# Optimization experiments

Measured on AMD Instinct MI355X. Metric: run time of the kernel, lower is better.

Reference implementation:

```python
import jax, jax.numpy as jnp
import numpy as np

K = 3          # kernel size
PAD = 1        # padding
KK = K * K
RECURRENT = 3  # opt.Recurrent_times - 1


def dcnv2(x, offset, mask, weight, bias):
    """Modulated deformable conv (DCNv2), stride 1, pad 1, dilation 1.

    x:      [B, C, H, W]
    offset: [B, 2*KK, H, W]  -- (dy, dx) interleaved per kernel tap
    mask:   [B, KK, H, W]    -- modulation scalars
    weight: [O, C, K, K], bias: [O]
    """
    B, C, H, W = x.shape
    off = offset.reshape(B, KK, 2, H, W)
    dy, dx = off[:, :, 0], off[:, :, 1]                       # [B,KK,H,W]

    ky, kx = jnp.meshgrid(jnp.arange(K), jnp.arange(K), indexing='ij')
    ky = (ky.reshape(KK) - PAD).astype(x.dtype)               # {-1,0,1}
    kx = (kx.reshape(KK) - PAD).astype(x.dtype)
    iy = jnp.arange(H, dtype=x.dtype)
    ix = jnp.arange(W, dtype=x.dtype)

    # fractional sampling coords, [B,KK,H,W]
    py = iy[None, None, :, None] + ky[None, :, None, None] + dy
    px = ix[None, None, None, :] + kx[None, :, None, None] + dx

    y0 = jnp.floor(py)
    x0 = jnp.floor(px)
    wy = (py - y0)[:, None]                                   # [B,1,KK,H,W]
    wx = (px - x0)[:, None]

    x_flat = x.reshape(B, C, H * W)

    def gather(yi, xi):
        valid = ((yi >= 0) & (yi <= H - 1) & (xi >= 0) & (xi <= W - 1))
        yc = jnp.clip(yi, 0, H - 1).astype(jnp.int32)
        xc = jnp.clip(xi, 0, W - 1).astype(jnp.int32)
        idx = (yc * W + xc).reshape(B, -1)                    # [B, KK*H*W]
        g = jax.vmap(lambda im, id_: im[:, id_])(x_flat, idx)  # [B,C,KK*H*W]
        return g.reshape(B, C, KK, H, W) * valid.astype(x.dtype)[:, None]

    v00 = gather(y0, x0)
    v01 = gather(y0, x0 + 1)
    v10 = gather(y0 + 1, x0)
    v11 = gather(y0 + 1, x0 + 1)

    val = (v00 * (1 - wy) * (1 - wx) + v01 * (1 - wy) * wx
           + v10 * wy * (1 - wx) + v11 * wy * wx)
    val = val * mask[:, None]                                  # modulation

    out = jnp.einsum('ock,bckhw->bohw', weight.reshape(weight.shape[0], C, KK), val)
    return out + bias[None, :, None, None]


def setup_inputs() -> dict:
    key = jax.random.key(0)
    k1, k2, k3 = jax.random.split(key, 3)
    B, H, W = 4, 512, 512
    sharp = jax.random.normal(k1, (B, 3, H, W), dtype=jnp.float32)
    motion = jax.random.normal(k2, (B, 3 * KK, H, W), dtype=jnp.float32)
    # one 3x3x3->3 conv per recurrence, stacked: [RECURRENT, O, C, K, K]
    dcn_weights = jax.random.normal(k3, (RECURRENT, 3, 3, K, K), dtype=jnp.float32) * 0.1
    dcn_biases = jnp.zeros((RECURRENT, 3), dtype=jnp.float32)
    return {"sharp": sharp, "motion": motion,
            "dcn_weights": dcn_weights, "dcn_biases": dcn_biases}


def reference(sharp, motion, dcn_weights, dcn_biases):
    # torch.split(motion, [2*KK, KK], dim=1)
    offset = motion[:, :2 * KK]
    mask = motion[:, 2 * KK:]
    feats = [sharp]
    cur = sharp
    for i in range(RECURRENT):
        cur = dcnv2(cur, offset, mask, dcn_weights[i], dcn_biases[i])
        feats.append(cur)
    return sum(feats) / (RECURRENT + 1)
```

## Files before the change

kernel.cpp:

```cpp
#include <hip/hip_runtime.h>
#include <hip/hip_fp16.h>


#define HH 512
#define WW 512
#define BATCH 4
#define HWSZ (HH * WW)
#define MP 28
#define MBLKS (108 * 256)

union U4 { uint4 u; __half2 h[4]; };
union U2 { uint2 u; __half2 h[2]; };

typedef const __attribute__((address_space(1))) void* gas_t;
typedef __attribute__((address_space(3))) void* las_t;

__global__ __launch_bounds__(256) void prep_kernel(
    const float* __restrict__ sharp, const float* __restrict__ motion,
    uint4* __restrict__ sharp16, __half* __restrict__ mot16)
{
    const int blk = blockIdx.x;
    const int t = threadIdx.x;
    if (blk < MBLKS) {
        const int P = blk >> 8;
        const int b = P / 27;
        const int pl = P - b * 27;
        const int off = (blk & 255) * 1024 + t * 4;
        const float4 v = *(const float4*)(motion + ((size_t)P << 18) + off);
        U2 o;
        o.h[0] = __float22half2_rn(make_float2(v.x, v.y));
        o.h[1] = __float22half2_rn(make_float2(v.z, v.w));
        *(uint2*)(mot16 + ((size_t)b * MP + pl) * HWSZ + off) = o.u;
    } else {
        const int i = (blk - MBLKS) * 256 + t;
        const int b = i >> 17;
        const int p = (i & (HWSZ / 2 - 1)) * 2;
        const float* s = sharp + (size_t)b * 3 * HWSZ + p;
        const float2 c0 = *(const float2*)(s);
        const float2 c1 = *(const float2*)(s + HWSZ);
        const float2 c2 = *(const float2*)(s + 2 * HWSZ);
        U4 o;
        o.h[0] = __float22half2_rn(make_float2(c0.x, c1.x));
        o.h[1] = __float22half2_rn(make_float2(c2.x, 0.f));
        o.h[2] = __float22half2_rn(make_float2(c0.y, c1.y));
        o.h[3] = __float22half2_rn(make_float2(c2.y, 0.f));
        sharp16[i] = o.u;
    }
}

__device__ __forceinline__ void bilinear3(const char* __restrict__ sb,
                                          float py, float px, float m,
                                          float& o0, float& o1, float& o2)
{
    const float y0f = floorf(py), x0f = floorf(px);
    const float wy = py - y0f, wx = px - x0f;
    const bool vy0 = (y0f >= 0.f) && (y0f <= 511.f);
    const bool vy1 = (y0f >= -1.f) && (y0f <= 510.f);
    const bool vx0 = (x0f >= 0.f) && (x0f <= 511.f);
    const bool vx1 = (x0f >= -1.f) && (x0f <= 510.f);
    const int iy0 = (int)fminf(fmaxf(y0f, 0.f), 511.f);
    const int iy1 = (int)fminf(fmaxf(y0f + 1.f, 0.f), 511.f);
    const int ix0 = (int)fminf(fmaxf(x0f, 0.f), 511.f);
    const int ix1 = (int)fminf(fmaxf(x0f + 1.f, 0.f), 511.f);
    const int lc  = (int)fminf(fmaxf(x0f, 0.f), 510.f);
    const int s0 = ix0 - lc;
    const int s1 = ix1 - lc;

    const float w00 = (vy0 && vx0) ? (1.f - wy) * (1.f - wx) * m : 0.f;
    const float w01 = (vy0 && vx1) ? (1.f - wy) * wx * m : 0.f;
    const float w10 = (vy1 && vx0) ? wy * (1.f - wx) * m : 0.f;
    const float w11 = (vy1 && vx1) ? wy * wx * m : 0.f;

    const float wlo0 = s0 ? 0.f : (s1 ? w00 : w00 + w01);
    const float whi0 = s1 ? (s0 ? w00 + w01 : w01) : 0.f;
    const float wlo1 = s0 ? 0.f : (s1 ? w10 : w10 + w11);
    const float whi1 = s1 ? (s0 ? w10 + w11 : w11) : 0.f;

    U4 ra, rb;
    ra.u = *(const uint4*)(sb + (size_t)(iy0 * WW + lc) * 8);
    rb.u = *(const uint4*)(sb + (size_t)(iy1 * WW + lc) * 8);
    const float2 aL = __half22float2(ra.h[0]);
    const float2 aLz = __half22float2(ra.h[1]);
    const float2 aH = __half22float2(ra.h[2]);
    const float2 aHz = __half22float2(ra.h[3]);
    const float2 bL = __half22float2(rb.h[0]);
    const float2 bLz = __half22float2(rb.h[1]);
    const float2 bH = __half22float2(rb.h[2]);
    const float2 bHz = __half22float2(rb.h[3]);

    o0 = wlo0 * aL.x + whi0 * aH.x + wlo1 * bL.x + whi1 * bH.x;
    o1 = wlo0 * aL.y + whi0 * aH.y + wlo1 * bL.y + whi1 * bH.y;
    o2 = wlo0 * aLz.x + whi0 * aHz.x + wlo1 * bLz.x + whi1 * bHz.x;
}

template <bool LAST>
__global__ __launch_bounds__(256) void dcn_kernel(
    const uint2* __restrict__ src,
    const __half* __restrict__ mot16,
    const float* __restrict__ wgt,
    const float* __restrict__ bias,
    uint2* __restrict__ dst,
    const uint2* __restrict__ cS,
    const uint2* __restrict__ c1,
    float* __restrict__ out)
{
    __shared__ __align__(16) char msmem[MP * 256 * 2];
    __shared__ float sw[84];

    const int t = threadIdx.x;
    const int blk = blockIdx.x;
    const int b = blk >> 10;
    const int pbase = (blk & 1023) * 256;
    const int y = pbase >> 9;
    const int x = (pbase & 511) + t;
    const int p = pbase + t;
    const int w = t >> 6, lane = t & 63;

    if (t < 84) sw[t] = (t < 81) ? wgt[t] : bias[t - 81];

    {
        const __half* mbase = mot16 + (size_t)b * MP * HWSZ + pbase;
#pragma unroll
        for (int r = 0; r < 4; ++r) {
            const int q = r * 4 + w;
            if (q < 14) {
                const int pl = 2 * q + (lane >> 5);
                const __half* gsrc = mbase + (size_t)pl * HWSZ + (lane & 31) * 8;
                __builtin_amdgcn_global_load_lds((gas_t)gsrc,
                                                 (las_t)(msmem + q * 1024),
                                                 16, 0, 0);
            }
        }
    }

    const uint2* simg = src + (size_t)b * HWSZ;

    U2 csv, c1v, c2v;
    if (LAST) {
        csv = *(const U2*)&cS[(size_t)b * HWSZ + p];
        c1v = *(const U2*)&c1[(size_t)b * HWSZ + p];
        c2v = *(const U2*)&simg[p];
    }

    __syncthreads();

    const char* sb = (const char*)simg;
    const __half* mh = (const __half*)msmem;
    float acc0 = sw[81], acc1 = sw[82], acc2 = sw[83];

#pragma unroll
    for (int k = 0; k < 9; ++k) {
        const float dy = __half2float(mh[(2 * k) * 256 + t]);
        const float dx = __half2float(mh[(2 * k + 1) * 256 + t]);
        const float m  = __half2float(mh[(18 + k) * 256 + t]);
        const float py = (float)(y + k / 3 - 1) + dy;
        const float px = (float)(x + k % 3 - 1) + dx;

        float v0, v1, v2;
        bilinear3(sb, py, px, m, v0, v1, v2);
        acc0 += sw[0 * 9 + k] * v0 + sw[1 * 9 + k] * v1 + sw[2 * 9 + k] * v2;
        acc1 += sw[3 * 9 + k] * v0 + sw[4 * 9 + k] * v1 + sw[5 * 9 + k] * v2;
        acc2 += sw[6 * 9 + k] * v0 + sw[7 * 9 + k] * v1 + sw[8 * 9 + k] * v2;
    }

    if (!LAST) {
        U2 o;
        o.h[0] = __float22half2_rn(make_float2(acc0, acc1));
        o.h[1] = __float22half2_rn(make_float2(acc2, 0.f));
        dst[(size_t)b * HWSZ + p] = o.u;
    } else {
        const float2 s01 = __half22float2(csv.h[0]);
        const float2 s2  = __half22float2(csv.h[1]);
        const float2 a01 = __half22float2(c1v.h[0]);
        const float2 a2  = __half22float2(c1v.h[1]);
        const float2 b01 = __half22float2(c2v.h[0]);
        const float2 b2  = __half22float2(c2v.h[1]);
        const size_t ob = (size_t)b * 3 * HWSZ + p;
        out[ob]            = (s01.x + a01.x + b01.x + acc0) * 0.25f;
        out[ob + HWSZ]     = (s01.y + a01.y + b01.y + acc1) * 0.25f;
        out[ob + 2 * HWSZ] = (s2.x  + a2.x  + b2.x  + acc2) * 0.25f;
    }
}

extern "C" void kernel_launch(void* const* d_in, const int* in_sizes, int n_in,
                              void* d_out, int out_size, void* d_ws, size_t ws_size,
                              hipStream_t stream) {
    const float* sharp  = (const float*)d_in[0];
    const float* motion = (const float*)d_in[1];
    const float* wts    = (const float*)d_in[2];
    const float* bias   = (const float*)d_in[3];
    float* out = (float*)d_out;

    const size_t img = (size_t)BATCH * HWSZ;
    uint2* bufS = (uint2*)d_ws;
    uint2* buf1 = bufS + img;
    uint2* buf2 = buf1 + img;
    __half* mot16 = (__half*)(buf2 + img);

    const dim3 block(256);
    const dim3 gridP(MBLKS + img / 512);
    const dim3 gridD(img / 256);

    prep_kernel<<<gridP, block, 0, stream>>>(sharp, motion, (uint4*)bufS, mot16);
    dcn_kernel<false><<<gridD, block, 0, stream>>>(
        bufS, mot16, wts, bias, buf1, nullptr, nullptr, nullptr);
    dcn_kernel<false><<<gridD, block, 0, stream>>>(
        buf1, mot16, wts + 81, bias + 3, buf2, nullptr, nullptr, nullptr);
    dcn_kernel<true><<<gridD, block, 0, stream>>>(
        buf2, mot16, wts + 162, bias + 6, nullptr, bufS, buf1, out);
}
```

Baseline: 125.3 us.

## Stage source halo tile in LDS and switch to 2D pixel blocks

Each block now covers a 4x64 pixel tile instead of a 256-pixel row segment, with blockIdx swizzled across batches. It preloads a 15x75 halo of the source image into shared memory, and samples whose footprint falls inside the tile read from LDS, with a global-memory fallback otherwise. The aim is to cut scattered global gathers by reusing neighbouring pixels. The cost is extra LDS traffic, halo loads that may go unused, and a divergent branch, since random offsets of unit variance may often land outside the halo.

New measurement: 181.3 us. +44.7%, slower.

```diff
diff --git a/kernel.cpp b/kernel.cpp
--- a/kernel.cpp
+++ b/kernel.cpp
@@ -8,6 +8,11 @@
 #define HWSZ (HH * WW)
 #define MP 28
 #define MBLKS (108 * 256)
+
+#define TROWS 15
+#define TCOLS 75
+#define HLY 5
+#define HLX 5
 
 union U4 { uint4 u; __half2 h[4]; };
 union U2 { uint2 u; __half2 h[2]; };
@@ -48,51 +53,6 @@
     }
 }
 
-__device__ __forceinline__ void bilinear3(const char* __restrict__ sb,
-                                          float py, float px, float m,
-                                          float& o0, float& o1, float& o2)
-{
-    const float y0f = floorf(py), x0f = floorf(px);
-    const float wy = py - y0f, wx = px - x0f;
-    const bool vy0 = (y0f >= 0.f) && (y0f <= 511.f);
-    const bool vy1 = (y0f >= -1.f) && (y0f <= 510.f);
-    const bool vx0 = (x0f >= 0.f) && (x0f <= 511.f);
-    const bool vx1 = (x0f >= -1.f) && (x0f <= 510.f);
-    const int iy0 = (int)fminf(fmaxf(y0f, 0.f), 511.f);
-    const int iy1 = (int)fminf(fmaxf(y0f + 1.f, 0.f), 511.f);
-    const int ix0 = (int)fminf(fmaxf(x0f, 0.f), 511.f);
-    const int ix1 = (int)fminf(fmaxf(x0f + 1.f, 0.f), 511.f);
-    const int lc  = (int)fminf(fmaxf(x0f, 0.f), 510.f);
-    const int s0 = ix0 - lc;
-    const int s1 = ix1 - lc;
-
-    const float w00 = (vy0 && vx0) ? (1.f - wy) * (1.f - wx) * m : 0.f;
-    const float w01 = (vy0 && vx1) ? (1.f - wy) * wx * m : 0.f;
-    const float w10 = (vy1 && vx0) ? wy * (1.f - wx) * m : 0.f;
-    const float w11 = (vy1 && vx1) ? wy * wx * m : 0.f;
-
-    const float wlo0 = s0 ? 0.f : (s1 ? w00 : w00 + w01);
-    const float whi0 = s1 ? (s0 ? w00 + w01 : w01) : 0.f;
-    const float wlo1 = s0 ? 0.f : (s1 ? w10 : w10 + w11);
-    const float whi1 = s1 ? (s0 ? w10 + w11 : w11) : 0.f;
-
-    U4 ra, rb;
-    ra.u = *(const uint4*)(sb + (size_t)(iy0 * WW + lc) * 8);
-    rb.u = *(const uint4*)(sb + (size_t)(iy1 * WW + lc) * 8);
-    const float2 aL = __half22float2(ra.h[0]);
-    const float2 aLz = __half22float2(ra.h[1]);
-    const float2 aH = __half22float2(ra.h[2]);
-    const float2 aHz = __half22float2(ra.h[3]);
-    const float2 bL = __half22float2(rb.h[0]);
-    const float2 bLz = __half22float2(rb.h[1]);
-    const float2 bH = __half22float2(rb.h[2]);
-    const float2 bHz = __half22float2(rb.h[3]);
-
-    o0 = wlo0 * aL.x + whi0 * aH.x + wlo1 * bL.x + whi1 * bH.x;
-    o1 = wlo0 * aL.y + whi0 * aH.y + wlo1 * bL.y + whi1 * bH.y;
-    o2 = wlo0 * aLz.x + whi0 * aHz.x + wlo1 * bLz.x + whi1 * bHz.x;
-}
-
 template <bool LAST>
 __global__ __launch_bounds__(256) void dcn_kernel(
     const uint2* __restrict__ src,
@@ -104,36 +64,51 @@
     const uint2* __restrict__ c1,
     float* __restrict__ out)
 {
-    __shared__ __align__(16) char msmem[MP * 256 * 2];
+    __shared__ __align__(16) __half msmem[MP * 256];
+    __shared__ U2 tile[TROWS * TCOLS];
     __shared__ float sw[84];
 
     const int t = threadIdx.x;
-    const int blk = blockIdx.x;
+    int blk = blockIdx.x;
+    blk = (blk & 7) * 512 + (blk >> 3);
     const int b = blk >> 10;
-    const int pbase = (blk & 1023) * 256;
-    const int y = pbase >> 9;
-    const int x = (pbase & 511) + t;
-    const int p = pbase + t;
+    const int tid = blk & 1023;
+    const int y0 = (tid >> 3) * 4;
+    const int x0 = (tid & 7) * 64;
     const int w = t >> 6, lane = t & 63;
+    const int y = y0 + w, x = x0 + lane;
+    const int p = y * WW + x;
 
     if (t < 84) sw[t] = (t < 81) ? wgt[t] : bias[t - 81];
 
     {
-        const __half* mbase = mot16 + (size_t)b * MP * HWSZ + pbase;
+        const __half* mb = mot16 + (size_t)b * MP * HWSZ + y0 * WW + x0;
 #pragma unroll
-        for (int r = 0; r < 4; ++r) {
-            const int q = r * 4 + w;
+        for (int rr = 0; rr < 4; ++rr) {
+            const int q = rr * 4 + w;
             if (q < 14) {
                 const int pl = 2 * q + (lane >> 5);
-                const __half* gsrc = mbase + (size_t)pl * HWSZ + (lane & 31) * 8;
+                const int l5 = lane & 31;
+                const __half* gsrc = mb + (size_t)pl * HWSZ + (l5 >> 3) * WW + (l5 & 7) * 8;
                 __builtin_amdgcn_global_load_lds((gas_t)gsrc,
-                                                 (las_t)(msmem + q * 1024),
+                                                 (las_t)(msmem + q * 512),
                                                  16, 0, 0);
             }
         }
     }
 
     const uint2* simg = src + (size_t)b * HWSZ;
+    const int rl = y0 - HLY, cl = x0 - HLX;
+#pragma unroll
+    for (int it = 0; it < 5; ++it) {
+        const int i = t + it * 256;
+        if (i < TROWS * TCOLS) {
+            const int rr = i / TCOLS, cc = i - rr * TCOLS;
+            const int gy = rl + rr, gx = cl + cc;
+            if (gy >= 0 && gy < HH && gx >= 0 && gx < WW)
+                tile[i] = *(const U2*)&simg[gy * WW + gx];
+        }
+    }
 
     U2 csv, c1v, c2v;
     if (LAST) {
@@ -145,19 +120,69 @@
     __syncthreads();
 
     const char* sb = (const char*)simg;
-    const __half* mh = (const __half*)msmem;
     float acc0 = sw[81], acc1 = sw[82], acc2 = sw[83];
 
 #pragma unroll
     for (int k = 0; k < 9; ++k) {
-        const float dy = __half2float(mh[(2 * k) * 256 + t]);
-        const float dx = __half2float(mh[(2 * k + 1) * 256 + t]);
-        const float m  = __half2float(mh[(18 + k) * 256 + t]);
+        const float dy = __half2float(msmem[(2 * k) * 256 + t]);
+        const float dx = __half2float(msmem[(2 * k + 1) * 256 + t]);
+        const float m  = __half2float(msmem[(18 + k) * 256 + t]);
         const float py = (float)(y + k / 3 - 1) + dy;
         const float px = (float)(x + k % 3 - 1) + dx;
 
-        float v0, v1, v2;
-        bilinear3(sb, py, px, m, v0, v1, v2);
+        const float y0f = floorf(py), x0f = floorf(px);
+        const float wy = py - y0f, wx = px - x0f;
+        const bool vy0 = (y0f >= 0.f) && (y0f <= 511.f);
+        const bool vy1 = (y0f >= -1.f) && (y0f <= 510.f);
+        const bool vx0 = (x0f >= 0.f) && (x0f <= 511.f);
+        const bool vx1 = (x0f >= -1.f) && (x0f <= 510.f);
+        const int iy0 = (int)fminf(fmaxf(y0f, 0.f), 511.f);
+        const int iy1 = (int)fminf(fmaxf(y0f + 1.f, 0.f), 511.f);
+        const int ix0 = (int)fminf(fmaxf(x0f, 0.f), 511.f);
+        const int ix1 = (int)fminf(fmaxf(x0f + 1.f, 0.f), 511.f);
+        const int lc  = (int)fminf(fmaxf(x0f, 0.f), 510.f);
+        const int s0 = ix0 - lc, s1 = ix1 - lc;
+
+        const float w00 = (vy0 && vx0) ? (1.f - wy) * (1.f - wx) * m : 0.f;
+        const float w01 = (vy0 && vx1) ? (1.f - wy) * wx * m : 0.f;
+        const float w10 = (vy1 && vx0) ? wy * (1.f - wx) * m : 0.f;
+        const float w11 = (vy1 && vx1) ? wy * wx * m : 0.f;
+        const float wlo0 = s0 ? 0.f : (s1 ? w00 : w00 + w01);
+        const float whi0 = s1 ? (s0 ? w00 + w01 : w01) : 0.f;
+        const float wlo1 = s0 ? 0.f : (s1 ? w10 : w10 + w11);
+        const float whi1 = s1 ? (s0 ? w10 + w11 : w11) : 0.f;
+
+        U2 aL, aH, bL, bH;
+        const bool fast = (iy0 >= rl) && (iy1 <= rl + TROWS - 1) &&
+                          (lc >= cl) && (lc <= cl + TCOLS - 2);
+        if (fast) {
+            const int ta = (iy0 - rl) * TCOLS + (lc - cl);
+            const int tb = (iy1 - rl) * TCOLS + (lc - cl);
+            aL = tile[ta]; aH = tile[ta + 1];
+            bL = tile[tb]; bH = tile[tb + 1];
+        } else {
+            U4 ra, rb;
+            ra.u = *(const uint4*)(sb + (size_t)(iy0 * WW + lc) * 8);
+            rb.u = *(const uint4*)(sb + (size_t)(iy1 * WW + lc) * 8);
+            aL.h[0] = ra.h[0]; aL.h[1] = ra.h[1];
+            aH.h[0] = ra.h[2]; aH.h[1] = ra.h[3];
+            bL.h[0] = rb.h[0]; bL.h[1] = rb.h[1];
+            bH.h[0] = rb.h[2]; bH.h[1] = rb.h[3];
+        }
+
+        const float2 aL01 = __half22float2(aL.h[0]);
+        const float2 aL2  = __half22float2(aL.h[1]);
+        const float2 aH01 = __half22float2(aH.h[0]);
+        const float2 aH2  = __half22float2(aH.h[1]);
+        const float2 bL01 = __half22float2(bL.h[0]);
+        const float2 bL2  = __half22float2(bL.h[1]);
+        const float2 bH01 = __half22float2(bH.h[0]);
+        const float2 bH2  = __half22float2(bH.h[1]);
+
+        const float v0 = wlo0 * aL01.x + whi0 * aH01.x + wlo1 * bL01.x + whi1 * bH01.x;
+        const float v1 = wlo0 * aL01.y + whi0 * aH01.y + wlo1 * bL01.y + whi1 * bH01.y;
+        const float v2 = wlo0 * aL2.x  + whi0 * aH2.x  + wlo1 * bL2.x  + whi1 * bH2.x;
+
         acc0 += sw[0 * 9 + k] * v0 + sw[1 * 9 + k] * v1 + sw[2 * 9 + k] * v2;
         acc1 += sw[3 * 9 + k] * v0 + sw[4 * 9 + k] * v1 + sw[5 * 9 + k] * v2;
         acc2 += sw[6 * 9 + k] * v0 + sw[7 * 9 + k] * v1 + sw[8 * 9 + k] * v2;
```

## Process one image row per block with row-major motion layout and XCD swizzle

Applied to the files above, without the earlier changes.

Each block now handles a full 512-pixel row, two pixels per thread. The fp16 motion buffer is re-laid out row-contiguous (27 planes × 512 per row) so each block fetches its offsets and masks with one contiguous global-to-LDS copy. Block indices are swizzled so that consecutive rows are spread across the 8 chiplets, aiming for better L2 locality of the neighbouring rows gathered. In exchange the block count is halved and each thread holds more registers, which may reduce occupancy.

New measurement: 130.1 us. 3.9% more time.

```diff
diff --git a/kernel.cpp b/kernel.cpp
--- a/kernel.cpp
+++ b/kernel.cpp
@@ -6,46 +6,46 @@
 #define WW 512
 #define BATCH 4
 #define HWSZ (HH * WW)
-#define MP 28
-#define MBLKS (108 * 256)
+#define NROWS (BATCH * HH)
+#define MROW (27 * 512)
 
 union U4 { uint4 u; __half2 h[4]; };
 union U2 { uint2 u; __half2 h[2]; };
 
 typedef const __attribute__((address_space(1))) void* gas_t;
 typedef __attribute__((address_space(3))) void* las_t;
+
+__device__ __forceinline__ int swz(int bid) {
+    return (bid & 7) * 256 + (bid >> 3);
+}
 
 __global__ __launch_bounds__(256) void prep_kernel(
     const float* __restrict__ sharp, const float* __restrict__ motion,
     uint4* __restrict__ sharp16, __half* __restrict__ mot16)
 {
-    const int blk = blockIdx.x;
+    const int r = swz(blockIdx.x);
     const int t = threadIdx.x;
-    if (blk < MBLKS) {
-        const int P = blk >> 8;
-        const int b = P / 27;
-        const int pl = P - b * 27;
-        const int off = (blk & 255) * 1024 + t * 4;
-        const float4 v = *(const float4*)(motion + ((size_t)P << 18) + off);
-        U2 o;
-        o.h[0] = __float22half2_rn(make_float2(v.x, v.y));
-        o.h[1] = __float22half2_rn(make_float2(v.z, v.w));
-        *(uint2*)(mot16 + ((size_t)b * MP + pl) * HWSZ + off) = o.u;
-    } else {
-        const int i = (blk - MBLKS) * 256 + t;
-        const int b = i >> 17;
-        const int p = (i & (HWSZ / 2 - 1)) * 2;
-        const float* s = sharp + (size_t)b * 3 * HWSZ + p;
-        const float2 c0 = *(const float2*)(s);
-        const float2 c1 = *(const float2*)(s + HWSZ);
-        const float2 c2 = *(const float2*)(s + 2 * HWSZ);
-        U4 o;
-        o.h[0] = __float22half2_rn(make_float2(c0.x, c1.x));
-        o.h[1] = __float22half2_rn(make_float2(c2.x, 0.f));
-        o.h[2] = __float22half2_rn(make_float2(c0.y, c1.y));
-        o.h[3] = __float22half2_rn(make_float2(c2.y, 0.f));
-        sharp16[i] = o.u;
-    }
+    const int b = r >> 9;
+    const int y = r & 511;
+
+    const float* msrc = motion + ((size_t)b * 27 << 18) + y * 512 + 2 * t;
+    __half2* mdst = (__half2*)(mot16 + (size_t)r * MROW) + t;
+#pragma unroll
+    for (int pl = 0; pl < 27; ++pl) {
+        const float2 v = *(const float2*)(msrc + ((size_t)pl << 18));
+        mdst[pl * 256] = __float22half2_rn(v);
+    }
+
+    const float* s = sharp + (size_t)b * 3 * HWSZ + y * 512 + 2 * t;
+    const float2 c0 = *(const float2*)(s);
+    const float2 c1 = *(const float2*)(s + HWSZ);
+    const float2 c2 = *(const float2*)(s + 2 * HWSZ);
+    U4 o;
+    o.h[0] = __float22half2_rn(make_float2(c0.x, c1.x));
+    o.h[1] = __float22half2_rn(make_float2(c2.x, 0.f));
+    o.h[2] = __float22half2_rn(make_float2(c0.y, c1.y));
+    o.h[3] = __float22half2_rn(make_float2(c2.y, 0.f));
+    sharp16[(size_t)r * 256 + t] = o.u;
 }
 
 __device__ __forceinline__ void bilinear3(const char* __restrict__ sb,
@@ -104,81 +104,105 @@
     const uint2* __restrict__ c1,
     float* __restrict__ out)
 {
-    __shared__ __align__(16) char msmem[MP * 256 * 2];
+    __shared__ __align__(16) __half mlds[MROW];
     __shared__ float sw[84];
 
     const int t = threadIdx.x;
-    const int blk = blockIdx.x;
-    const int b = blk >> 10;
-    const int pbase = (blk & 1023) * 256;
-    const int y = pbase >> 9;
-    const int x = (pbase & 511) + t;
-    const int p = pbase + t;
+    const int r = swz(blockIdx.x);
+    const int b = r >> 9;
+    const int y = r & 511;
     const int w = t >> 6, lane = t & 63;
+    const int p1 = r * 512 + t;
+    const int p2 = p1 + 256;
 
     if (t < 84) sw[t] = (t < 81) ? wgt[t] : bias[t - 81];
 
     {
-        const __half* mbase = mot16 + (size_t)b * MP * HWSZ + pbase;
+        const __half* mrow = mot16 + (size_t)r * MROW;
 #pragma unroll
-        for (int r = 0; r < 4; ++r) {
-            const int q = r * 4 + w;
-            if (q < 14) {
-                const int pl = 2 * q + (lane >> 5);
-                const __half* gsrc = mbase + (size_t)pl * HWSZ + (lane & 31) * 8;
-                __builtin_amdgcn_global_load_lds((gas_t)gsrc,
-                                                 (las_t)(msmem + q * 1024),
+        for (int i = 0; i < 7; ++i) {
+            const int c = i * 4 + w;
+            if (c < 27) {
+                __builtin_amdgcn_global_load_lds((gas_t)(mrow + c * 512 + lane * 8),
+                                                 (las_t)(mlds + c * 512),
                                                  16, 0, 0);
             }
         }
     }
 
-    const uint2* simg = src + (size_t)b * HWSZ;
-
-    U2 csv, c1v, c2v;
+    const uint2* simg = src + ((size_t)b << 18);
+
+    U2 csA, c1A, c2A, csB, c1B, c2B;
     if (LAST) {
-        csv = *(const U2*)&cS[(size_t)b * HWSZ + p];
-        c1v = *(const U2*)&c1[(size_t)b * HWSZ + p];
-        c2v = *(const U2*)&simg[p];
+        csA = *(const U2*)&cS[p1];  csB = *(const U2*)&cS[p2];
+        c1A = *(const U2*)&c1[p1];  c1B = *(const U2*)&c1[p2];
+        c2A = *(const U2*)&src[p1]; c2B = *(const U2*)&src[p2];
     }
 
     __syncthreads();
 
     const char* sb = (const char*)simg;
-    const __half* mh = (const __half*)msmem;
-    float acc0 = sw[81], acc1 = sw[82], acc2 = sw[83];
+    float a00 = sw[81], a01 = sw[82], a02 = sw[83];
+    float a10 = sw[81], a11 = sw[82], a12 = sw[83];
 
 #pragma unroll
     for (int k = 0; k < 9; ++k) {
-        const float dy = __half2float(mh[(2 * k) * 256 + t]);
-        const float dx = __half2float(mh[(2 * k + 1) * 256 + t]);
-        const float m  = __half2float(mh[(18 + k) * 256 + t]);
-        const float py = (float)(y + k / 3 - 1) + dy;
-        const float px = (float)(x + k % 3 - 1) + dx;
+        const float ky = (float)(y + k / 3 - 1);
+        const float kxA = (float)(t + k % 3 - 1);
+        const float kxB = kxA + 256.f;
+
+        const float dyA = __half2float(mlds[(2 * k) * 512 + t]);
+        const float dxA = __half2float(mlds[(2 * k + 1) * 512 + t]);
+        const float mA  = __half2float(mlds[(18 + k) * 512 + t]);
+        const float dyB = __half2float(mlds[(2 * k) * 512 + t + 256]);
+        const float dxB = __half2float(mlds[(2 * k + 1) * 512 + t + 256]);
+        const float mB  = __half2float(mlds[(18 + k) * 512 + t + 256]);
 
         float v0, v1, v2;
-        bilinear3(sb, py, px, m, v0, v1, v2);
-        acc0 += sw[0 * 9 + k] * v0 + sw[1 * 9 + k] * v1 + sw[2 * 9 + k] * v2;
-        acc1 += sw[3 * 9 + k] * v0 + sw[4 * 9 + k] * v1 + sw[5 * 9 + k] * v2;
-        acc2 += sw[6 * 9 + k] * v0 + sw[7 * 9 + k] * v1 + sw[8 * 9 + k] * v2;
+        bilinear3(sb, ky + dyA, kxA + dxA, mA, v0, v1, v2);
+        a00 += sw[0 * 9 + k] * v0 + sw[1 * 9 + k] * v1 + sw[2 * 9 + k] * v2;
+        a01 += sw[3 * 9 + k] * v0 + sw[4 * 9 + k] * v1 + sw[5 * 9 + k] * v2;
+        a02 += sw[6 * 9 + k] * v0 + sw[7 * 9 + k] * v1 + sw[8 * 9 + k] * v2;
+
+        float u0, u1, u2;
+        bilinear3(sb, ky + dyB, kxB + dxB, mB, u0, u1, u2);
+        a10 += sw[0 * 9 + k] * u0 + sw[1 * 9 + k] * u1 + sw[2 * 9 + k] * u2;
+        a11 += sw[3 * 9 + k] * u0 + sw[4 * 9 + k] * u1 + sw[5 * 9 + k] * u2;
+        a12 += sw[6 * 9 + k] * u0 + sw[7 * 9 + k] * u1 + sw[8 * 9 + k] * u2;
     }
 
     if (!LAST) {
-        U2 o;
-        o.h[0] = __float22half2_rn(make_float2(acc0, acc1));
-        o.h[1] = __float22half2_rn(make_float2(acc2, 0.f));
-        dst[(size_t)b * HWSZ + p] = o.u;
+        U2 oA, oB;
+        oA.h[0] = __float22half2_rn(make_float2(a00, a01));
+        oA.h[1] = __float22half2_rn(make_float2(a02, 0.f));
+        oB.h[0] = __float22half2_rn(make_float2(a10, a11));
+        oB.h[1] = __float22half2_rn(make_float2(a12, 0.f));
+        dst[p1] = oA.u;
+        dst[p2] = oB.u;
     } else {
-        const float2 s01 = __half22float2(csv.h[0]);
-        const float2 s2  = __half22float2(csv.h[1]);
-        const float2 a01 = __half22float2(c1v.h[0]);
-        const float2 a2  = __half22float2(c1v.h[1]);
-        const float2 b01 = __half22float2(c2v.h[0]);
-        const float2 b2  = __half22float2(c2v.h[1]);
-        const size_t ob = (size_t)b * 3 * HWSZ + p;
-        out[ob]            = (s01.x + a01.x + b01.x + acc0) * 0.25f;
-        out[ob + HWSZ]     = (s01.y + a01.y + b01.y + acc1) * 0.25f;
-        out[ob + 2 * HWSZ] = (s2.x  + a2.x  + b2.x  + acc2) * 0.25f;
+        const size_t ob = (size_t)b * 3 * HWSZ + y * 512 + t;
+        {
+            const float2 s01 = __half22float2(csA.h[0]);
+            const float2 s2  = __half22float2(csA.h[1]);
+            const float2 f101 = __half22float2(c1A.h[0]);
+            const float2 f12  = __half22float2(c1A.h[1]);
+            const float2 f201 = __half22float2(c2A.h[0]);
+            const float2 f22  = __half22float2(c2A.h[1]);
+            out[ob]            = (s01.x + f101.x + f201.x + a00) * 0.25f;
+            out[ob + HWSZ]     = (s01.y + f101.y + f201.y + a01) * 0.25f;
+            out[ob + 2 * HWSZ] = (s2.x  + f12.x  + f22.x  + a02) * 0.25f;
+        }
+        {
+            const float2 s01 = __half22float2(csB.h[0]);
+            const float2 s2  = __half22float2(csB.h[1]);
+            const float2 f101 = __half22float2(c1B.h[0]);
+            const float2 f12  = __half22float2(c1B.h[1]);
+            const float2 f201 = __half22float2(c2B.h[0]);
+            const float2 f22  = __half22float2(c2B.h[1]);
+            out[ob + 256]            = (s01.x + f101.x + f201.x + a10) * 0.25f;
+            out[ob + 256 + HWSZ]     = (s01.y + f101.y + f201.y + a11) * 0.25f;
+            out[ob + 256 + 2 * HWSZ] = (s2.x  + f12.x  + f22.x  + a12) * 0.25f;
+        }
     }
 }
 
@@ -192,20 +216,19 @@
     float* out = (float*)d_out;
 
     const size_t img = (size_t)BATCH * HWSZ;
-    uint2* bufS = (uint2*)d_ws;
+    __half* mot16 = (__half*)d_ws;
+    uint2* bufS = (uint2*)(mot16 + (size_t)NROWS * MROW);
     uint2* buf1 = bufS + img;
     uint2* buf2 = buf1 + img;
-    __half* mot16 = (__half*)(buf2 + img);
 
     const dim3 block(256);
-    const dim3 gridP(MBLKS + img / 512);
-    const dim3 gridD(img / 256);
-
-    prep_kernel<<<gridP, block, 0, stream>>>(sharp, motion, (uint4*)bufS, mot16);
-    dcn_kernel<false><<<gridD, block, 0, stream>>>(
+    const dim3 grid(NROWS);
+
+    prep_kernel<<<grid, block, 0, stream>>>(sharp, motion, (uint4*)bufS, mot16);
+    dcn_kernel<false><<<grid, block, 0, stream>>>(
         bufS, mot16, wts, bias, buf1, nullptr, nullptr, nullptr);
-    dcn_kernel<false><<<gridD, block, 0, stream>>>(
+    dcn_kernel<false><<<grid, block, 0, stream>>>(
         buf1, mot16, wts + 81, bias + 3, buf2, nullptr, nullptr, nullptr);
-    dcn_kernel<true><<<gridD, block, 0, stream>>>(
+    dcn_kernel<true><<<grid, block, 0, stream>>>(
         buf2, mot16, wts + 162, bias + 6, nullptr, bufS, buf1, out);
 }
```

## Precompute bilinear tap offsets and weights once, reuse across three DCN passes

Applied to the files above, without the earlier changes.

The prep kernel now computes, for each pixel and tap, a packed gather offset and the fp16 bilinear weights with the mask folded in, and stores them in a per-block strip layout. The three DCN passes load these precomputed taps into LDS and skip coordinate, validity and weight math, leaving only the gathers and FMAs. Per-pass input traffic stays about the same size as the old fp16 motion planes (27 KB per block), so the gain comes from dropping repeated ALU work. The cost is that the prep kernel reads fp32 motion directly and does the tap math once. The weights now carry extra fp16 rounding.

Result: slower. 134.8 us (+7.5%).

```diff
diff --git a/kernel.cpp b/kernel.cpp
--- a/kernel.cpp
+++ b/kernel.cpp
@@ -6,8 +6,8 @@
 #define WW 512
 #define BATCH 4
 #define HWSZ (HH * WW)
-#define MP 28
-#define MBLKS (108 * 256)
+#define NSTRIP 4096
+#define TAPB 27648
 
 union U4 { uint4 u; __half2 h[4]; };
 union U2 { uint2 u; __half2 h[2]; };
@@ -17,22 +17,14 @@
 
 __global__ __launch_bounds__(256) void prep_kernel(
     const float* __restrict__ sharp, const float* __restrict__ motion,
-    uint4* __restrict__ sharp16, __half* __restrict__ mot16)
+    uint4* __restrict__ sharp16, char* __restrict__ taps)
 {
+    __shared__ __align__(16) char msmem[27 * 1024];
+    const int t = threadIdx.x;
     const int blk = blockIdx.x;
-    const int t = threadIdx.x;
-    if (blk < MBLKS) {
-        const int P = blk >> 8;
-        const int b = P / 27;
-        const int pl = P - b * 27;
-        const int off = (blk & 255) * 1024 + t * 4;
-        const float4 v = *(const float4*)(motion + ((size_t)P << 18) + off);
-        U2 o;
-        o.h[0] = __float22half2_rn(make_float2(v.x, v.y));
-        o.h[1] = __float22half2_rn(make_float2(v.z, v.w));
-        *(uint2*)(mot16 + ((size_t)b * MP + pl) * HWSZ + off) = o.u;
-    } else {
-        const int i = (blk - MBLKS) * 256 + t;
+
+    if (blk >= NSTRIP) {
+        const int i = (blk - NSTRIP) * 256 + t;
         const int b = i >> 17;
         const int p = (i & (HWSZ / 2 - 1)) * 2;
         const float* s = sharp + (size_t)b * 3 * HWSZ + p;
@@ -45,58 +37,73 @@
         o.h[2] = __float22half2_rn(make_float2(c0.y, c1.y));
         o.h[3] = __float22half2_rn(make_float2(c2.y, 0.f));
         sharp16[i] = o.u;
-    }
-}
-
-__device__ __forceinline__ void bilinear3(const char* __restrict__ sb,
-                                          float py, float px, float m,
-                                          float& o0, float& o1, float& o2)
-{
-    const float y0f = floorf(py), x0f = floorf(px);
-    const float wy = py - y0f, wx = px - x0f;
-    const bool vy0 = (y0f >= 0.f) && (y0f <= 511.f);
-    const bool vy1 = (y0f >= -1.f) && (y0f <= 510.f);
-    const bool vx0 = (x0f >= 0.f) && (x0f <= 511.f);
-    const bool vx1 = (x0f >= -1.f) && (x0f <= 510.f);
-    const int iy0 = (int)fminf(fmaxf(y0f, 0.f), 511.f);
-    const int iy1 = (int)fminf(fmaxf(y0f + 1.f, 0.f), 511.f);
-    const int ix0 = (int)fminf(fmaxf(x0f, 0.f), 511.f);
-    const int ix1 = (int)fminf(fmaxf(x0f + 1.f, 0.f), 511.f);
-    const int lc  = (int)fminf(fmaxf(x0f, 0.f), 510.f);
-    const int s0 = ix0 - lc;
-    const int s1 = ix1 - lc;
-
-    const float w00 = (vy0 && vx0) ? (1.f - wy) * (1.f - wx) * m : 0.f;
-    const float w01 = (vy0 && vx1) ? (1.f - wy) * wx * m : 0.f;
-    const float w10 = (vy1 && vx0) ? wy * (1.f - wx) * m : 0.f;
-    const float w11 = (vy1 && vx1) ? wy * wx * m : 0.f;
-
-    const float wlo0 = s0 ? 0.f : (s1 ? w00 : w00 + w01);
-    const float whi0 = s1 ? (s0 ? w00 + w01 : w01) : 0.f;
-    const float wlo1 = s0 ? 0.f : (s1 ? w10 : w10 + w11);
-    const float whi1 = s1 ? (s0 ? w10 + w11 : w11) : 0.f;
-
-    U4 ra, rb;
-    ra.u = *(const uint4*)(sb + (size_t)(iy0 * WW + lc) * 8);
-    rb.u = *(const uint4*)(sb + (size_t)(iy1 * WW + lc) * 8);
-    const float2 aL = __half22float2(ra.h[0]);
-    const float2 aLz = __half22float2(ra.h[1]);
-    const float2 aH = __half22float2(ra.h[2]);
-    const float2 aHz = __half22float2(ra.h[3]);
-    const float2 bL = __half22float2(rb.h[0]);
-    const float2 bLz = __half22float2(rb.h[1]);
-    const float2 bH = __half22float2(rb.h[2]);
-    const float2 bHz = __half22float2(rb.h[3]);
-
-    o0 = wlo0 * aL.x + whi0 * aH.x + wlo1 * bL.x + whi1 * bH.x;
-    o1 = wlo0 * aL.y + whi0 * aH.y + wlo1 * bL.y + whi1 * bH.y;
-    o2 = wlo0 * aLz.x + whi0 * aHz.x + wlo1 * bLz.x + whi1 * bHz.x;
+        return;
+    }
+
+    const int b = blk >> 10;
+    const int pbase = (blk & 1023) * 256;
+    const int y = pbase >> 9;
+    const int x = (pbase & 511) + t;
+    const int w = t >> 6, lane = t & 63;
+
+    {
+        const float* mbase = motion + (size_t)b * 27 * HWSZ + pbase;
+#pragma unroll
+        for (int r = 0; r < 7; ++r) {
+            const int pl = r * 4 + w;
+            if (pl < 27) {
+                __builtin_amdgcn_global_load_lds((gas_t)(mbase + (size_t)pl * HWSZ + lane * 4),
+                                                 (las_t)(msmem + pl * 1024),
+                                                 16, 0, 0);
+            }
+        }
+    }
+    __syncthreads();
+
+    const float* mf = (const float*)msmem;
+    char* tb = taps + (size_t)blk * TAPB;
+
+#pragma unroll
+    for (int k = 0; k < 9; ++k) {
+        const float dy = mf[(2 * k) * 256 + t];
+        const float dx = mf[(2 * k + 1) * 256 + t];
+        const float m  = mf[(18 + k) * 256 + t];
+        const float py = (float)(y + k / 3 - 1) + dy;
+        const float px = (float)(x + k % 3 - 1) + dx;
+
+        const float y0f = floorf(py), x0f = floorf(px);
+        const float wy = py - y0f, wx = px - x0f;
+        const bool vy0 = (y0f >= 0.f) && (y0f <= 511.f);
+        const bool vy1 = (y0f >= -1.f) && (y0f <= 510.f);
+        const bool vx0 = (x0f >= 0.f) && (x0f <= 511.f);
+        const bool vx1 = (x0f >= -1.f) && (x0f <= 510.f);
+        const int iy0 = (int)fminf(fmaxf(y0f, 0.f), 511.f);
+        const int iy1 = (int)fminf(fmaxf(y0f + 1.f, 0.f), 511.f);
+        const int ix0 = (int)fminf(fmaxf(x0f, 0.f), 511.f);
+        const int ix1 = (int)fminf(fmaxf(x0f + 1.f, 0.f), 511.f);
+        const int lc  = (int)fminf(fmaxf(x0f, 0.f), 510.f);
+        const int s0 = ix0 - lc, s1 = ix1 - lc;
+
+        const float w00 = (vy0 && vx0) ? (1.f - wy) * (1.f - wx) * m : 0.f;
+        const float w01 = (vy0 && vx1) ? (1.f - wy) * wx * m : 0.f;
+        const float w10 = (vy1 && vx0) ? wy * (1.f - wx) * m : 0.f;
+        const float w11 = (vy1 && vx1) ? wy * wx * m : 0.f;
+        const float wlo0 = s0 ? 0.f : (s1 ? w00 : w00 + w01);
+        const float whi0 = s1 ? (s0 ? w00 + w01 : w01) : 0.f;
+        const float wlo1 = s0 ? 0.f : (s1 ? w10 : w10 + w11);
+        const float whi1 = s1 ? (s0 ? w10 + w11 : w11) : 0.f;
+
+        const unsigned off = ((unsigned)((iy0 << 9) | lc) << 1) | (unsigned)(iy1 != iy0);
+        *(unsigned*)(tb + k * 1024 + t * 4) = off;
+        *(__half2*)(tb + 9216 + k * 1024 + t * 4)  = __float22half2_rn(make_float2(wlo0, whi0));
+        *(__half2*)(tb + 18432 + k * 1024 + t * 4) = __float22half2_rn(make_float2(wlo1, whi1));
+    }
 }
 
 template <bool LAST>
 __global__ __launch_bounds__(256) void dcn_kernel(
     const uint2* __restrict__ src,
-    const __half* __restrict__ mot16,
+    const char* __restrict__ taps,
     const float* __restrict__ wgt,
     const float* __restrict__ bias,
     uint2* __restrict__ dst,
@@ -104,60 +111,73 @@
     const uint2* __restrict__ c1,
     float* __restrict__ out)
 {
-    __shared__ __align__(16) char msmem[MP * 256 * 2];
+    __shared__ __align__(16) char msmem[TAPB];
     __shared__ float sw[84];
 
     const int t = threadIdx.x;
     const int blk = blockIdx.x;
     const int b = blk >> 10;
     const int pbase = (blk & 1023) * 256;
-    const int y = pbase >> 9;
-    const int x = (pbase & 511) + t;
     const int p = pbase + t;
     const int w = t >> 6, lane = t & 63;
 
     if (t < 84) sw[t] = (t < 81) ? wgt[t] : bias[t - 81];
 
     {
-        const __half* mbase = mot16 + (size_t)b * MP * HWSZ + pbase;
-#pragma unroll
-        for (int r = 0; r < 4; ++r) {
-            const int q = r * 4 + w;
-            if (q < 14) {
-                const int pl = 2 * q + (lane >> 5);
-                const __half* gsrc = mbase + (size_t)pl * HWSZ + (lane & 31) * 8;
-                __builtin_amdgcn_global_load_lds((gas_t)gsrc,
-                                                 (las_t)(msmem + q * 1024),
+        const char* tb = taps + (size_t)blk * TAPB;
+#pragma unroll
+        for (int r = 0; r < 7; ++r) {
+            const int pl = r * 4 + w;
+            if (pl < 27) {
+                __builtin_amdgcn_global_load_lds((gas_t)(tb + pl * 1024 + lane * 16),
+                                                 (las_t)(msmem + pl * 1024),
                                                  16, 0, 0);
             }
         }
     }
 
-    const uint2* simg = src + (size_t)b * HWSZ;
+    const uint2* simg = src + ((size_t)b << 18);
 
     U2 csv, c1v, c2v;
     if (LAST) {
-        csv = *(const U2*)&cS[(size_t)b * HWSZ + p];
-        c1v = *(const U2*)&c1[(size_t)b * HWSZ + p];
+        csv = *(const U2*)&cS[((size_t)b << 18) + p];
+        c1v = *(const U2*)&c1[((size_t)b << 18) + p];
         c2v = *(const U2*)&simg[p];
     }
 
     __syncthreads();
 
     const char* sb = (const char*)simg;
-    const __half* mh = (const __half*)msmem;
+    const unsigned* offs = (const unsigned*)msmem;
+    const __half2* w0 = (const __half2*)(msmem + 9216);
+    const __half2* w1 = (const __half2*)(msmem + 18432);
+
     float acc0 = sw[81], acc1 = sw[82], acc2 = sw[83];
 
 #pragma unroll
     for (int k = 0; k < 9; ++k) {
-        const float dy = __half2float(mh[(2 * k) * 256 + t]);
-        const float dx = __half2float(mh[(2 * k + 1) * 256 + t]);
-        const float m  = __half2float(mh[(18 + k) * 256 + t]);
-        const float py = (float)(y + k / 3 - 1) + dy;
-        const float px = (float)(x + k % 3 - 1) + dx;
-
-        float v0, v1, v2;
-        bilinear3(sb, py, px, m, v0, v1, v2);
+        const unsigned off = offs[k * 256 + t];
+        const float2 wA = __half22float2(w0[k * 256 + t]);
+        const float2 wB = __half22float2(w1[k * 256 + t]);
+
+        const char* pa = sb + (size_t)(off >> 1) * 8;
+        U4 ra, rb;
+        ra.u = *(const uint4*)(pa);
+        rb.u = *(const uint4*)(pa + (off & 1) * 4096);
+
+        const float2 aL01 = __half22float2(ra.h[0]);
+        const float2 aL2  = __half22float2(ra.h[1]);
+        const float2 aH01 = __half22float2(ra.h[2]);
+        const float2 aH2  = __half22float2(ra.h[3]);
+        const float2 bL01 = __half22float2(rb.h[0]);
+        const float2 bL2  = __half22float2(rb.h[1]);
+        const float2 bH01 = __half22float2(rb.h[2]);
+        const float2 bH2  = __half22float2(rb.h[3]);
+
+        const float v0 = wA.x * aL01.x + wA.y * aH01.x + wB.x * bL01.x + wB.y * bH01.x;
+        const float v1 = wA.x * aL01.y + wA.y * aH01.y + wB.x * bL01.y + wB.y * bH01.y;
+        const float v2 = wA.x * aL2.x  + wA.y * aH2.x  + wB.x * bL2.x  + wB.y * bH2.x;
+
         acc0 += sw[0 * 9 + k] * v0 + sw[1 * 9 + k] * v1 + sw[2 * 9 + k] * v2;
         acc1 += sw[3 * 9 + k] * v0 + sw[4 * 9 + k] * v1 + sw[5 * 9 + k] * v2;
         acc2 += sw[6 * 9 + k] * v0 + sw[7 * 9 + k] * v1 + sw[8 * 9 + k] * v2;
@@ -167,7 +187,7 @@
         U2 o;
         o.h[0] = __float22half2_rn(make_float2(acc0, acc1));
         o.h[1] = __float22half2_rn(make_float2(acc2, 0.f));
-        dst[(size_t)b * HWSZ + p] = o.u;
+        dst[((size_t)b << 18) + p] = o.u;
     } else {
         const float2 s01 = __half22float2(csv.h[0]);
         const float2 s2  = __half22float2(csv.h[1]);
@@ -192,20 +212,20 @@
     float* out = (float*)d_out;
 
     const size_t img = (size_t)BATCH * HWSZ;
-    uint2* bufS = (uint2*)d_ws;
+    char* taps = (char*)d_ws;
+    uint2* bufS = (uint2*)(taps + (size_t)NSTRIP * TAPB);
     uint2* buf1 = bufS + img;
     uint2* buf2 = buf1 + img;
-    __half* mot16 = (__half*)(buf2 + img);
 
     const dim3 block(256);
-    const dim3 gridP(MBLKS + img / 512);
-    const dim3 gridD(img / 256);
-
-    prep_kernel<<<gridP, block, 0, stream>>>(sharp, motion, (uint4*)bufS, mot16);
+    const dim3 gridP(NSTRIP + 2048);
+    const dim3 gridD(NSTRIP);
+
+    prep_kernel<<<gridP, block, 0, stream>>>(sharp, motion, (uint4*)bufS, taps);
     dcn_kernel<false><<<gridD, block, 0, stream>>>(
-        bufS, mot16, wts, bias, buf1, nullptr, nullptr, nullptr);
+        bufS, taps, wts, bias, buf1, nullptr, nullptr, nullptr);
     dcn_kernel<false><<<gridD, block, 0, stream>>>(
-        buf1, mot16, wts + 81, bias + 3, buf2, nullptr, nullptr, nullptr);
+        buf1, taps, wts + 81, bias + 3, buf2, nullptr, nullptr, nullptr);
     dcn_kernel<true><<<gridD, block, 0, stream>>>(
-        buf2, mot16, wts + 162, bias + 6, nullptr, bufS, buf1, out);
+        buf2, taps, wts + 162, bias + 6, nullptr, bufS, buf1, out);
 }
```
